# Kernel optimization log

Measured on AMD Instinct MI355X. Metric: run time of the kernel, lower is better.

Reference implementation:

```python
import jax, jax.numpy as jnp
import numpy as np

C = 256
HEAD_DIM = 8
N_HEAD = C // HEAD_DIM  # 32
GN_GROUPS = max(1, C // 32)  # 8
GN_EPS = 1e-5


def setup_inputs() -> dict:
    key = jax.random.key(0)
    ks = jax.random.split(key, 7)
    x = jax.random.normal(ks[0], (8, C, 32, 32), dtype=jnp.float32)
    gn_w = jax.random.normal(ks[1], (C,), dtype=jnp.float32) * 0.02 + 1.0
    gn_b = jax.random.normal(ks[2], (C,), dtype=jnp.float32) * 0.02
    qkv_w = jax.random.normal(ks[3], (3 * C, C), dtype=jnp.float32) / np.sqrt(C)
    qkv_b = jax.random.normal(ks[4], (3 * C,), dtype=jnp.float32) * 0.01
    out_w = jax.random.normal(ks[5], (C, C), dtype=jnp.float32) / np.sqrt(C)
    out_b = jax.random.normal(ks[6], (C,), dtype=jnp.float32) * 0.01
    return {"x": x, "gn_w": gn_w, "gn_b": gn_b, "qkv_w": qkv_w,
            "qkv_b": qkv_b, "out_w": out_w, "out_b": out_b}


def reference(x, gn_w, gn_b, qkv_w, qkv_b, out_w, out_b):
    n, c, h, w = x.shape
    hw = h * w
    # --- GroupNorm ---
    xg = x.reshape(n, GN_GROUPS, c // GN_GROUPS * hw)
    mu = jnp.mean(xg, axis=-1, keepdims=True)
    var = jnp.var(xg, axis=-1, keepdims=True)
    xn = ((xg - mu) * jax.lax.rsqrt(var + GN_EPS)).reshape(n, c, hw)
    xn = xn * gn_w[None, :, None] + gn_b[None, :, None]
    # --- QKV 1x1 conv ---
    qkv = jnp.einsum('oc,nct->not', qkv_w, xn) + qkv_b[None, :, None]  # [n,3c,hw]
    qkv = qkv.reshape(n, 3, N_HEAD, HEAD_DIM, hw)
    q, k, v = qkv[:, 0], qkv[:, 1], qkv[:, 2]  # each [n, heads, hd, hw]
    # --- attention over hw tokens ---
    scale = 1.0 / np.sqrt(HEAD_DIM)
    att = jnp.einsum('nhds,nhdt->nhst', q, k) * scale  # [n,heads,hw,hw]
    att = jax.nn.softmax(att, axis=-1)
    y = jnp.einsum('nhst,nhdt->nhds', att, v)  # [n,heads,hd,hw]
    y = y.reshape(n, c, hw)
    # --- output 1x1 conv + residual ---
    out = jnp.einsum('oc,nct->not', out_w, y) + out_b[None, :, None]
    return x + out.reshape(n, c, h, w)
```

## Files before the change

### kernel.cpp

```cpp
#include <hip/hip_runtime.h>
#include <hip/hip_bf16.h>
#include <math.h>


#define NBATCH 8
#define C 256
#define HW 1024
#define NHEAD 32
#define HDIM 8

typedef __bf16 bf16x8 __attribute__((ext_vector_type(8)));
typedef __bf16 bf16x4 __attribute__((ext_vector_type(4)));
typedef _Float16 f16x8 __attribute__((ext_vector_type(8)));
typedef _Float16 f16x4 __attribute__((ext_vector_type(4)));
typedef float floatx4 __attribute__((ext_vector_type(4)));
typedef float floatx16 __attribute__((ext_vector_type(16)));

#if __has_builtin(__builtin_amdgcn_exp2f)
#define EXP2F(x) __builtin_amdgcn_exp2f(x)
#else
#define EXP2F(x) exp2f(x)
#endif

#define SCALE_LOG2E 0.51013249662f

__global__ __launch_bounds__(256) void gn_stats_cvt_kernel(
    const float* __restrict__ x, float* __restrict__ stats,
    const float* __restrict__ qw, const float* __restrict__ ow,
    __bf16* __restrict__ wq, __bf16* __restrict__ wo)
{
    int blk = blockIdx.x;
    int tid = threadIdx.x;
    if (blk >= 512) {
        int id = (blk - 512) * 256 + tid;
        float4 v;
        __bf16* dst;
        if (id < 49152) { v = *(const float4*)&qw[id * 4]; dst = wq + id * 4; }
        else { v = *(const float4*)&ow[(id - 49152) * 4]; dst = wo + (id - 49152) * 4; }
        bf16x4 o = { (__bf16)v.x, (__bf16)v.y, (__bf16)v.z, (__bf16)v.w };
        *(bf16x4*)dst = o;
        return;
    }
    int part = blk & 7, ng = blk >> 3;
    const float4* xv = (const float4*)(x + ((size_t)ng * 32 + part * 4) * HW);
    float s = 0.f, ss = 0.f;
#pragma unroll
    for (int i = 0; i < 4; ++i) {
        float4 v = xv[tid + i * 256];
        s  += v.x + v.y + v.z + v.w;
        ss += v.x*v.x + v.y*v.y + v.z*v.z + v.w*v.w;
    }
#pragma unroll
    for (int o = 32; o; o >>= 1) { s += __shfl_xor(s, o); ss += __shfl_xor(ss, o); }
    __shared__ float rs[4], rss[4];
    int wave = tid >> 6, lane = tid & 63;
    if (lane == 0) { rs[wave] = s; rss[wave] = ss; }
    __syncthreads();
    if (tid == 0) {
        stats[blk * 2]     = rs[0] + rs[1] + rs[2] + rs[3];
        stats[blk * 2 + 1] = rss[0] + rss[1] + rss[2] + rss[3];
    }
}

__global__ __launch_bounds__(256) void gn_apply_kernel(
    const float* __restrict__ x, const float* __restrict__ w,
    const float* __restrict__ b, const float* __restrict__ stats,
    __bf16* __restrict__ xnT)
{
    int blk = blockIdx.x;
    int chunk = blk & 3, ng = blk >> 2;
    int n = ng >> 3, g = ng & 7;
    float s = 0.f, ss = 0.f;
#pragma unroll
    for (int p = 0; p < 8; ++p) {
        s  += stats[(ng * 8 + p) * 2];
        ss += stats[(ng * 8 + p) * 2 + 1];
    }
    const float invN = 1.0f / 32768.0f;
    float mean = s * invN;
    float var  = ss * invN - mean * mean;
    float rstd = rsqrtf(var + 1e-5f);
    const float* xp = x + ((size_t)ng * 32) * HW;
    int tid = threadIdx.x, t0 = chunk * 256;
    __shared__ __bf16 Lt[32][257];
#pragma unroll 8
    for (int c = 0; c < 32; ++c) {
        float wc = w[g * 32 + c] * rstd;
        float bc = b[g * 32 + c] - mean * wc;
        float v = xp[(size_t)c * HW + t0 + tid];
        Lt[c][tid] = (__bf16)(v * wc + bc);
    }
    __syncthreads();
    __bf16* xo = xnT + (size_t)n * HW * C + g * 32;
#pragma unroll
    for (int q = 0; q < 4; ++q) {
        bf16x8 o;
#pragma unroll
        for (int e = 0; e < 8; ++e) o[e] = Lt[q * 8 + e][tid];
        *(bf16x8*)&xo[(size_t)(t0 + tid) * C + q * 8] = o;
    }
}

__global__ __launch_bounds__(256) void gemm_qkv_kernel(
    const __bf16* __restrict__ W, const __bf16* __restrict__ Ball,
    const float* __restrict__ bias, _Float16* __restrict__ Qf,
    _Float16* __restrict__ Kf, __bf16* __restrict__ Vbf)
{
    int n = blockIdx.z;
    const __bf16* B = Ball + (size_t)n * HW * C;
    int om0 = blockIdx.y * 64, t0 = blockIdx.x * 128;
    __shared__ __bf16 As[64 * 32];
    __shared__ __bf16 Bs[128 * 32];
    int tid = threadIdx.x, lane = tid & 63, wave = tid >> 6;
    int l15 = lane & 15, quad = lane >> 4;
    int wm = (wave & 1) * 32, wn = (wave >> 1) * 64;
    int swq = (quad ^ (l15 & 3)) * 8;
    int arow = tid >> 2, aq = tid & 3;
    int sw = (aq ^ (arow & 3)) * 8;
    floatx4 acc[2][4] = {};
    for (int c0 = 0; c0 < C; c0 += 32) {
        bf16x8 av  = *(const bf16x8*)&W[(size_t)(om0 + arow) * C + c0 + aq * 8];
        bf16x8 bv0 = *(const bf16x8*)&B[(size_t)(t0 + arow) * C + c0 + aq * 8];
        bf16x8 bv1 = *(const bf16x8*)&B[(size_t)(t0 + 64 + arow) * C + c0 + aq * 8];
        __syncthreads();
        *(bf16x8*)&As[arow * 32 + sw] = av;
        *(bf16x8*)&Bs[arow * 32 + sw] = bv0;
        *(bf16x8*)&Bs[(arow + 64) * 32 + sw] = bv1;
        __syncthreads();
        bf16x8 af[2], bfr[4];
#pragma unroll
        for (int mi = 0; mi < 2; ++mi)
            af[mi] = *(const bf16x8*)&As[(wm + mi * 16 + l15) * 32 + swq];
#pragma unroll
        for (int ni = 0; ni < 4; ++ni)
            bfr[ni] = *(const bf16x8*)&Bs[(wn + ni * 16 + l15) * 32 + swq];
#pragma unroll
        for (int mi = 0; mi < 2; ++mi)
#pragma unroll
            for (int ni = 0; ni < 4; ++ni)
                acc[mi][ni] = __builtin_amdgcn_mfma_f32_16x16x32_bf16(
                    af[mi], bfr[ni], acc[mi][ni], 0, 0, 0);
    }
#pragma unroll
    for (int mi = 0; mi < 2; ++mi) {
        int obase = om0 + wm + mi * 16;
        int oq = obase + quad * 4;
        if (obase < 512) {
            int h  = (oq & 255) >> 3;
            int d0 = (quad & 1) * 4;
            _Float16* dst = (obase < 256 ? Qf : Kf);
            float mul = (obase < 256) ? SCALE_LOG2E : 1.0f;
#pragma unroll
            for (int ni = 0; ni < 4; ++ni) {
                int t = t0 + wn + ni * 16 + l15;
                f16x4 o;
#pragma unroll
                for (int r = 0; r < 4; ++r)
                    o[r] = (_Float16)((acc[mi][ni][r] + bias[oq + r]) * mul);
                *(f16x4*)&dst[(((size_t)(n * 32 + h)) * HW + t) * 8 + d0] = o;
            }
        } else {
            int cv = oq - 512;
#pragma unroll
            for (int ni = 0; ni < 4; ++ni) {
                int t = t0 + wn + ni * 16 + l15;
#pragma unroll
                for (int r = 0; r < 4; ++r)
                    Vbf[((size_t)(n * 256 + cv + r)) * HW + t] =
                        (__bf16)(acc[mi][ni][r] + bias[oq + r]);
            }
        }
    }
}

__global__ __launch_bounds__(256) void gemm_out_kernel(
    const __bf16* __restrict__ W, const __bf16* __restrict__ Ball,
    const float* __restrict__ bias, float* __restrict__ Call,
    const float* __restrict__ Rall)
{
    int n = blockIdx.z;
    const __bf16* B = Ball + (size_t)n * HW * C;
    float* Cp = Call + (size_t)n * C * HW;
    const float* R = Rall + (size_t)n * C * HW;
    int om0 = blockIdx.y * 64, t0 = blockIdx.x * 64;
    __shared__ __bf16 As[64 * 32];
    __shared__ __bf16 Bs[64 * 32];
    int tid = threadIdx.x, lane = tid & 63, wave = tid >> 6;
    int l15 = lane & 15, quad = lane >> 4;
    int wm = (wave & 1) * 32, wn = (wave >> 1) * 32;
    int swq = (quad ^ (l15 & 3)) * 8;
    int arow = tid >> 2, aq = tid & 3;
    int sw = (aq ^ (arow & 3)) * 8;
    floatx4 acc[2][2] = {};
    for (int c0 = 0; c0 < C; c0 += 32) {
        bf16x8 av = *(const bf16x8*)&W[(size_t)(om0 + arow) * C + c0 + aq * 8];
        bf16x8 bv = *(const bf16x8*)&B[(size_t)(t0 + arow) * C + c0 + aq * 8];
        __syncthreads();
        *(bf16x8*)&As[arow * 32 + sw] = av;
        *(bf16x8*)&Bs[arow * 32 + sw] = bv;
        __syncthreads();
        bf16x8 af[2], bfr[2];
#pragma unroll
        for (int mi = 0; mi < 2; ++mi)
            af[mi] = *(const bf16x8*)&As[(wm + mi * 16 + l15) * 32 + swq];
#pragma unroll
        for (int ni = 0; ni < 2; ++ni)
            bfr[ni] = *(const bf16x8*)&Bs[(wn + ni * 16 + l15) * 32 + swq];
#pragma unroll
        for (int mi = 0; mi < 2; ++mi)
#pragma unroll
            for (int ni = 0; ni < 2; ++ni)
                acc[mi][ni] = __builtin_amdgcn_mfma_f32_16x16x32_bf16(
                    af[mi], bfr[ni], acc[mi][ni], 0, 0, 0);
    }
#pragma unroll
    for (int mi = 0; mi < 2; ++mi) {
#pragma unroll
        for (int r = 0; r < 4; ++r) {
            int o = om0 + wm + mi * 16 + quad * 4 + r;
            float bb = bias[o];
#pragma unroll
            for (int ni = 0; ni < 2; ++ni) {
                int t = t0 + wn + ni * 16 + l15;
                Cp[(size_t)o * HW + t] = acc[mi][ni][r] + bb + R[(size_t)o * HW + t];
            }
        }
    }
}

__global__ __launch_bounds__(256, 4) void attn_kernel(
    const _Float16* __restrict__ Qf, const _Float16* __restrict__ Kf,
    const __bf16* __restrict__ Vg, __bf16* __restrict__ yT)
{
    int quarter = blockIdx.x & 3, h = (blockIdx.x >> 2) & 31, n = blockIdx.x >> 7;
    __shared__ alignas(16) _Float16 Kb[HW][8];
    __shared__ alignas(16) __bf16   Vb[9][HW + 8];
    int tid = threadIdx.x;
    const _Float16* kg = Kf + ((size_t)(n * 32 + h)) * HW * 8;
    const __bf16*   vg = Vg + ((size_t)(n * 256 + h * 8)) * HW;
#pragma unroll
    for (int i = 0; i < 4; ++i) {
        int row = tid + i * 256;
        *(f16x8*)&Kb[row][0] = *(const f16x8*)&kg[(size_t)row * 8];
    }
#pragma unroll
    for (int i = 0; i < 4; ++i) {
        int id = tid + i * 256;
        int d = id >> 7, t8 = (id & 127) * 8;
        *(bf16x8*)&Vb[d][t8] = *(const bf16x8*)&vg[(size_t)d * HW + t8];
    }
    if (tid < 128) {
        __bf16 one = (__bf16)1.0f;
        bf16x8 ones = { one, one, one, one, one, one, one, one };
        *(bf16x8*)&Vb[8][tid * 8] = ones;
    }
    int lane = tid & 63, wave = tid >> 6;
    int l31 = lane & 31, lhi = lane >> 5;
    int vrow = l31 < 9 ? l31 : (l31 & 7);
    const __bf16* vbase = &Vb[vrow][0];
    int tqb = quarter * 256 + wave * 64;
    const _Float16* qg = Qf + ((size_t)(n * 32 + h)) * HW * 8;
    f16x8 qf[2];
#pragma unroll
    for (int tau = 0; tau < 2; ++tau) {
        f16x8 qv = { 0, 0, 0, 0, 0, 0, 0, 0 };
        if (lhi == 0)
            qv = *(const f16x8*)&qg[(size_t)(tqb + tau * 32 + l31) * 8];
        qf[tau] = qv;
    }
    __syncthreads();
    floatx16 accG[2] = {};
    floatx16 zero16 = {};
    for (int tkt = 0; tkt < 32; ++tkt) {
        f16x8 kf = *(const f16x8*)&Kb[tkt * 32 + l31][0];
        int cb = tkt * 32 + lhi * 4;
        bf16x4 va0 = *(const bf16x4*)&vbase[cb];
        bf16x4 va1 = *(const bf16x4*)&vbase[cb + 8];
        bf16x4 va2 = *(const bf16x4*)&vbase[cb + 16];
        bf16x4 va3 = *(const bf16x4*)&vbase[cb + 24];
        bf16x8 vf0 = __builtin_shufflevector(va0, va1, 0, 1, 2, 3, 4, 5, 6, 7);
        bf16x8 vf1 = __builtin_shufflevector(va2, va3, 0, 1, 2, 3, 4, 5, 6, 7);
#pragma unroll
        for (int tau = 0; tau < 2; ++tau) {
            floatx16 sT = __builtin_amdgcn_mfma_f32_32x32x16_f16(
                kf, qf[tau], zero16, 0, 0, 0);
            __bf16 p[16];
#pragma unroll
            for (int r = 0; r < 16; ++r) p[r] = (__bf16)EXP2F(sT[r]);
            bf16x8 P0 = { p[0], p[1], p[2], p[3], p[4], p[5], p[6], p[7] };
            bf16x8 P1 = { p[8], p[9], p[10], p[11], p[12], p[13], p[14], p[15] };
            accG[tau] = __builtin_amdgcn_mfma_f32_32x32x16_bf16(
                vf0, P0, accG[tau], 0, 0, 0);
            accG[tau] = __builtin_amdgcn_mfma_f32_32x32x16_bf16(
                vf1, P1, accG[tau], 0, 0, 0);
        }
    }
    __bf16* yp = yT + (size_t)n * HW * C + h * HDIM + lhi * 4;
#pragma unroll
    for (int tau = 0; tau < 2; ++tau) {
        float own4 = accG[tau][4];
        float part4 = __shfl_xor(own4, 32);
        float lsum = lhi ? part4 : own4;
        float inv = 1.0f / lsum;
        bf16x4 o = { (__bf16)(accG[tau][0] * inv), (__bf16)(accG[tau][1] * inv),
                     (__bf16)(accG[tau][2] * inv), (__bf16)(accG[tau][3] * inv) };
        *(bf16x4*)&yp[(size_t)(tqb + tau * 32 + l31) * C] = o;
    }
}

extern "C" void kernel_launch(void* const* d_in, const int* in_sizes, int n_in,
                              void* d_out, int out_size, void* d_ws, size_t ws_size,
                              hipStream_t stream)
{
    const float* x     = (const float*)d_in[0];
    const float* gn_w  = (const float*)d_in[1];
    const float* gn_b  = (const float*)d_in[2];
    const float* qkv_w = (const float*)d_in[3];
    const float* qkv_b = (const float*)d_in[4];
    const float* out_w = (const float*)d_in[5];
    const float* out_b = (const float*)d_in[6];
    float* out = (float*)d_out;

    char* wsb = (char*)d_ws;
    __bf16*   xnT = (__bf16*)wsb;
    _Float16* Qf  = (_Float16*)(wsb + ((size_t)4 << 20));
    _Float16* Kf  = (_Float16*)(wsb + ((size_t)8 << 20));
    __bf16*   Vbf = (__bf16*)(wsb + ((size_t)12 << 20));
    __bf16*   yTp = (__bf16*)(wsb + ((size_t)16 << 20));
    __bf16*   wq  = (__bf16*)(wsb + ((size_t)20 << 20));
    __bf16*   wo  = wq + (size_t)3 * C * C;
    float*    st  = (float*)(wsb + ((size_t)21 << 20));

    gn_stats_cvt_kernel<<<768, 256, 0, stream>>>(x, st, qkv_w, out_w, wq, wo);
    gn_apply_kernel<<<256, 256, 0, stream>>>(x, gn_w, gn_b, st, xnT);
    gemm_qkv_kernel<<<dim3(8, 12, 8), 256, 0, stream>>>(wq, xnT, qkv_b,
                                                        Qf, Kf, Vbf);
    attn_kernel<<<1024, 256, 0, stream>>>(Qf, Kf, Vbf, yTp);
    gemm_out_kernel<<<dim3(16, 4, 8), 256, 0, stream>>>(wo, yTp, out_b, out, x);
}
```

Baseline: 125.4 us.

## Drop LDS staging in attention, read K/V from global and double block count

New measurement: 215.5 us. 1.72x slower.

```diff
diff --git a/kernel.cpp b/kernel.cpp
--- a/kernel.cpp
+++ b/kernel.cpp
@@ -27,12 +27,18 @@
 __global__ __launch_bounds__(256) void gn_stats_cvt_kernel(
     const float* __restrict__ x, float* __restrict__ stats,
     const float* __restrict__ qw, const float* __restrict__ ow,
-    __bf16* __restrict__ wq, __bf16* __restrict__ wo)
+    __bf16* __restrict__ wq, __bf16* __restrict__ wo,
+    __bf16* __restrict__ onesG)
 {
     int blk = blockIdx.x;
     int tid = threadIdx.x;
     if (blk >= 512) {
         int id = (blk - 512) * 256 + tid;
+        if (blk == 512 && tid < 128) {
+            __bf16 one = (__bf16)1.0f;
+            bf16x8 ones = { one, one, one, one, one, one, one, one };
+            *(bf16x8*)&onesG[tid * 8] = ones;
+        }
         float4 v;
         __bf16* dst;
         if (id < 49152) { v = *(const float4*)&qw[id * 4]; dst = wq + id * 4; }
@@ -228,84 +234,51 @@
     }
 }
 
-__global__ __launch_bounds__(256, 4) void attn_kernel(
+__global__ __launch_bounds__(256, 8) void attn_kernel(
     const _Float16* __restrict__ Qf, const _Float16* __restrict__ Kf,
-    const __bf16* __restrict__ Vg, __bf16* __restrict__ yT)
-{
-    int quarter = blockIdx.x & 3, h = (blockIdx.x >> 2) & 31, n = blockIdx.x >> 7;
-    __shared__ alignas(16) _Float16 Kb[HW][8];
-    __shared__ alignas(16) __bf16   Vb[9][HW + 8];
-    int tid = threadIdx.x;
+    const __bf16* __restrict__ Vg, const __bf16* __restrict__ onesG,
+    __bf16* __restrict__ yT)
+{
+    int eighth = blockIdx.x & 7, h = (blockIdx.x >> 3) & 31, n = blockIdx.x >> 8;
+    int tid = threadIdx.x, lane = tid & 63, wave = tid >> 6;
+    int l31 = lane & 31, lhi = lane >> 5;
     const _Float16* kg = Kf + ((size_t)(n * 32 + h)) * HW * 8;
     const __bf16*   vg = Vg + ((size_t)(n * 256 + h * 8)) * HW;
-#pragma unroll
-    for (int i = 0; i < 4; ++i) {
-        int row = tid + i * 256;
-        *(f16x8*)&Kb[row][0] = *(const f16x8*)&kg[(size_t)row * 8];
-    }
-#pragma unroll
-    for (int i = 0; i < 4; ++i) {
-        int id = tid + i * 256;
-        int d = id >> 7, t8 = (id & 127) * 8;
-        *(bf16x8*)&Vb[d][t8] = *(const bf16x8*)&vg[(size_t)d * HW + t8];
-    }
-    if (tid < 128) {
-        __bf16 one = (__bf16)1.0f;
-        bf16x8 ones = { one, one, one, one, one, one, one, one };
-        *(bf16x8*)&Vb[8][tid * 8] = ones;
-    }
-    int lane = tid & 63, wave = tid >> 6;
-    int l31 = lane & 31, lhi = lane >> 5;
-    int vrow = l31 < 9 ? l31 : (l31 & 7);
-    const __bf16* vbase = &Vb[vrow][0];
-    int tqb = quarter * 256 + wave * 64;
+    const __bf16* vrow = (l31 == 8) ? onesG : (vg + (size_t)(l31 & 7) * HW);
+    int tq0 = eighth * 128 + wave * 32;
     const _Float16* qg = Qf + ((size_t)(n * 32 + h)) * HW * 8;
-    f16x8 qf[2];
-#pragma unroll
-    for (int tau = 0; tau < 2; ++tau) {
-        f16x8 qv = { 0, 0, 0, 0, 0, 0, 0, 0 };
-        if (lhi == 0)
-            qv = *(const f16x8*)&qg[(size_t)(tqb + tau * 32 + l31) * 8];
-        qf[tau] = qv;
-    }
-    __syncthreads();
-    floatx16 accG[2] = {};
+    f16x8 qf = { 0, 0, 0, 0, 0, 0, 0, 0 };
+    if (lhi == 0)
+        qf = *(const f16x8*)&qg[(size_t)(tq0 + l31) * 8];
+    floatx16 acc = {};
     floatx16 zero16 = {};
     for (int tkt = 0; tkt < 32; ++tkt) {
-        f16x8 kf = *(const f16x8*)&Kb[tkt * 32 + l31][0];
+        f16x8 kf = *(const f16x8*)&kg[(size_t)(tkt * 32 + l31) * 8];
         int cb = tkt * 32 + lhi * 4;
-        bf16x4 va0 = *(const bf16x4*)&vbase[cb];
-        bf16x4 va1 = *(const bf16x4*)&vbase[cb + 8];
-        bf16x4 va2 = *(const bf16x4*)&vbase[cb + 16];
-        bf16x4 va3 = *(const bf16x4*)&vbase[cb + 24];
+        bf16x4 va0 = *(const bf16x4*)&vrow[cb];
+        bf16x4 va1 = *(const bf16x4*)&vrow[cb + 8];
+        bf16x4 va2 = *(const bf16x4*)&vrow[cb + 16];
+        bf16x4 va3 = *(const bf16x4*)&vrow[cb + 24];
         bf16x8 vf0 = __builtin_shufflevector(va0, va1, 0, 1, 2, 3, 4, 5, 6, 7);
         bf16x8 vf1 = __builtin_shufflevector(va2, va3, 0, 1, 2, 3, 4, 5, 6, 7);
-#pragma unroll
-        for (int tau = 0; tau < 2; ++tau) {
-            floatx16 sT = __builtin_amdgcn_mfma_f32_32x32x16_f16(
-                kf, qf[tau], zero16, 0, 0, 0);
-            __bf16 p[16];
-#pragma unroll
-            for (int r = 0; r < 16; ++r) p[r] = (__bf16)EXP2F(sT[r]);
-            bf16x8 P0 = { p[0], p[1], p[2], p[3], p[4], p[5], p[6], p[7] };
-            bf16x8 P1 = { p[8], p[9], p[10], p[11], p[12], p[13], p[14], p[15] };
-            accG[tau] = __builtin_amdgcn_mfma_f32_32x32x16_bf16(
-                vf0, P0, accG[tau], 0, 0, 0);
-            accG[tau] = __builtin_amdgcn_mfma_f32_32x32x16_bf16(
-                vf1, P1, accG[tau], 0, 0, 0);
-        }
+        floatx16 sT = __builtin_amdgcn_mfma_f32_32x32x16_f16(
+            kf, qf, zero16, 0, 0, 0);
+        __bf16 p[16];
+#pragma unroll
+        for (int r = 0; r < 16; ++r) p[r] = (__bf16)EXP2F(sT[r]);
+        bf16x8 P0 = { p[0], p[1], p[2], p[3], p[4], p[5], p[6], p[7] };
+        bf16x8 P1 = { p[8], p[9], p[10], p[11], p[12], p[13], p[14], p[15] };
+        acc = __builtin_amdgcn_mfma_f32_32x32x16_bf16(vf0, P0, acc, 0, 0, 0);
+        acc = __builtin_amdgcn_mfma_f32_32x32x16_bf16(vf1, P1, acc, 0, 0, 0);
     }
     __bf16* yp = yT + (size_t)n * HW * C + h * HDIM + lhi * 4;
-#pragma unroll
-    for (int tau = 0; tau < 2; ++tau) {
-        float own4 = accG[tau][4];
-        float part4 = __shfl_xor(own4, 32);
-        float lsum = lhi ? part4 : own4;
-        float inv = 1.0f / lsum;
-        bf16x4 o = { (__bf16)(accG[tau][0] * inv), (__bf16)(accG[tau][1] * inv),
-                     (__bf16)(accG[tau][2] * inv), (__bf16)(accG[tau][3] * inv) };
-        *(bf16x4*)&yp[(size_t)(tqb + tau * 32 + l31) * C] = o;
-    }
+    float own4 = acc[4];
+    float part4 = __shfl_xor(own4, 32);
+    float lsum = lhi ? part4 : own4;
+    float inv = 1.0f / lsum;
+    bf16x4 o = { (__bf16)(acc[0] * inv), (__bf16)(acc[1] * inv),
+                 (__bf16)(acc[2] * inv), (__bf16)(acc[3] * inv) };
+    *(bf16x4*)&yp[(size_t)(tq0 + l31) * C] = o;
 }
 
 extern "C" void kernel_launch(void* const* d_in, const int* in_sizes, int n_in,
@@ -330,11 +303,13 @@
     __bf16*   wq  = (__bf16*)(wsb + ((size_t)20 << 20));
     __bf16*   wo  = wq + (size_t)3 * C * C;
     float*    st  = (float*)(wsb + ((size_t)21 << 20));
-
-    gn_stats_cvt_kernel<<<768, 256, 0, stream>>>(x, st, qkv_w, out_w, wq, wo);
+    __bf16*   ones = (__bf16*)(wsb + ((size_t)21 << 20) + 8192);
+
+    gn_stats_cvt_kernel<<<768, 256, 0, stream>>>(x, st, qkv_w, out_w, wq, wo,
+                                                 ones);
     gn_apply_kernel<<<256, 256, 0, stream>>>(x, gn_w, gn_b, st, xnT);
     gemm_qkv_kernel<<<dim3(8, 12, 8), 256, 0, stream>>>(wq, xnT, qkv_b,
                                                         Qf, Kf, Vbf);
-    attn_kernel<<<1024, 256, 0, stream>>>(Qf, Kf, Vbf, yTp);
+    attn_kernel<<<2048, 256, 0, stream>>>(Qf, Kf, Vbf, ones, yTp);
     gemm_out_kernel<<<dim3(16, 4, 8), 256, 0, stream>>>(wo, yTp, out_b, out, x);
 }
```

## Load GEMM MFMA fragments directly from global memory, dropping LDS staging

Applied to the files above, without the earlier changes.

Result: slower. 137.9 us (+9.9%).

```diff
diff --git a/kernel.cpp b/kernel.cpp
--- a/kernel.cpp
+++ b/kernel.cpp
@@ -109,37 +109,33 @@
     int n = blockIdx.z;
     const __bf16* B = Ball + (size_t)n * HW * C;
     int om0 = blockIdx.y * 64, t0 = blockIdx.x * 128;
-    __shared__ __bf16 As[64 * 32];
-    __shared__ __bf16 Bs[128 * 32];
     int tid = threadIdx.x, lane = tid & 63, wave = tid >> 6;
     int l15 = lane & 15, quad = lane >> 4;
     int wm = (wave & 1) * 32, wn = (wave >> 1) * 64;
-    int swq = (quad ^ (l15 & 3)) * 8;
-    int arow = tid >> 2, aq = tid & 3;
-    int sw = (aq ^ (arow & 3)) * 8;
+    const __bf16* ap0 = &W[(size_t)(om0 + wm + l15) * C + quad * 8];
+    const __bf16* ap1 = ap0 + (size_t)16 * C;
+    const __bf16* bp0 = &B[(size_t)(t0 + wn + l15) * C + quad * 8];
+    const __bf16* bp1 = bp0 + (size_t)16 * C;
+    const __bf16* bp2 = bp0 + (size_t)32 * C;
+    const __bf16* bp3 = bp0 + (size_t)48 * C;
     floatx4 acc[2][4] = {};
-    for (int c0 = 0; c0 < C; c0 += 32) {
-        bf16x8 av  = *(const bf16x8*)&W[(size_t)(om0 + arow) * C + c0 + aq * 8];
-        bf16x8 bv0 = *(const bf16x8*)&B[(size_t)(t0 + arow) * C + c0 + aq * 8];
-        bf16x8 bv1 = *(const bf16x8*)&B[(size_t)(t0 + 64 + arow) * C + c0 + aq * 8];
-        __syncthreads();
-        *(bf16x8*)&As[arow * 32 + sw] = av;
-        *(bf16x8*)&Bs[arow * 32 + sw] = bv0;
-        *(bf16x8*)&Bs[(arow + 64) * 32 + sw] = bv1;
-        __syncthreads();
-        bf16x8 af[2], bfr[4];
-#pragma unroll
-        for (int mi = 0; mi < 2; ++mi)
-            af[mi] = *(const bf16x8*)&As[(wm + mi * 16 + l15) * 32 + swq];
-#pragma unroll
-        for (int ni = 0; ni < 4; ++ni)
-            bfr[ni] = *(const bf16x8*)&Bs[(wn + ni * 16 + l15) * 32 + swq];
-#pragma unroll
-        for (int mi = 0; mi < 2; ++mi)
-#pragma unroll
-            for (int ni = 0; ni < 4; ++ni)
-                acc[mi][ni] = __builtin_amdgcn_mfma_f32_16x16x32_bf16(
-                    af[mi], bfr[ni], acc[mi][ni], 0, 0, 0);
+#pragma unroll
+    for (int k = 0; k < 8; ++k) {
+        int c0 = k * 32;
+        bf16x8 af0 = *(const bf16x8*)&ap0[c0];
+        bf16x8 af1 = *(const bf16x8*)&ap1[c0];
+        bf16x8 bf0 = *(const bf16x8*)&bp0[c0];
+        bf16x8 bf1 = *(const bf16x8*)&bp1[c0];
+        bf16x8 bf2 = *(const bf16x8*)&bp2[c0];
+        bf16x8 bf3 = *(const bf16x8*)&bp3[c0];
+        acc[0][0] = __builtin_amdgcn_mfma_f32_16x16x32_bf16(af0, bf0, acc[0][0], 0, 0, 0);
+        acc[0][1] = __builtin_amdgcn_mfma_f32_16x16x32_bf16(af0, bf1, acc[0][1], 0, 0, 0);
+        acc[0][2] = __builtin_amdgcn_mfma_f32_16x16x32_bf16(af0, bf2, acc[0][2], 0, 0, 0);
+        acc[0][3] = __builtin_amdgcn_mfma_f32_16x16x32_bf16(af0, bf3, acc[0][3], 0, 0, 0);
+        acc[1][0] = __builtin_amdgcn_mfma_f32_16x16x32_bf16(af1, bf0, acc[1][0], 0, 0, 0);
+        acc[1][1] = __builtin_amdgcn_mfma_f32_16x16x32_bf16(af1, bf1, acc[1][1], 0, 0, 0);
+        acc[1][2] = __builtin_amdgcn_mfma_f32_16x16x32_bf16(af1, bf2, acc[1][2], 0, 0, 0);
+        acc[1][3] = __builtin_amdgcn_mfma_f32_16x16x32_bf16(af1, bf3, acc[1][3], 0, 0, 0);
     }
 #pragma unroll
     for (int mi = 0; mi < 2; ++mi) {
@@ -183,35 +179,25 @@
     float* Cp = Call + (size_t)n * C * HW;
     const float* R = Rall + (size_t)n * C * HW;
     int om0 = blockIdx.y * 64, t0 = blockIdx.x * 64;
-    __shared__ __bf16 As[64 * 32];
-    __shared__ __bf16 Bs[64 * 32];
     int tid = threadIdx.x, lane = tid & 63, wave = tid >> 6;
     int l15 = lane & 15, quad = lane >> 4;
     int wm = (wave & 1) * 32, wn = (wave >> 1) * 32;
-    int swq = (quad ^ (l15 & 3)) * 8;
-    int arow = tid >> 2, aq = tid & 3;
-    int sw = (aq ^ (arow & 3)) * 8;
+    const __bf16* ap0 = &W[(size_t)(om0 + wm + l15) * C + quad * 8];
+    const __bf16* ap1 = ap0 + (size_t)16 * C;
+    const __bf16* bp0 = &B[(size_t)(t0 + wn + l15) * C + quad * 8];
+    const __bf16* bp1 = bp0 + (size_t)16 * C;
     floatx4 acc[2][2] = {};
-    for (int c0 = 0; c0 < C; c0 += 32) {
-        bf16x8 av = *(const bf16x8*)&W[(size_t)(om0 + arow) * C + c0 + aq * 8];
-        bf16x8 bv = *(const bf16x8*)&B[(size_t)(t0 + arow) * C + c0 + aq * 8];
-        __syncthreads();
-        *(bf16x8*)&As[arow * 32 + sw] = av;
-        *(bf16x8*)&Bs[arow * 32 + sw] = bv;
-        __syncthreads();
-        bf16x8 af[2], bfr[2];
-#pragma unroll
-        for (int mi = 0; mi < 2; ++mi)
-            af[mi] = *(const bf16x8*)&As[(wm + mi * 16 + l15) * 32 + swq];
-#pragma unroll
-        for (int ni = 0; ni < 2; ++ni)
-            bfr[ni] = *(const bf16x8*)&Bs[(wn + ni * 16 + l15) * 32 + swq];
-#pragma unroll
-        for (int mi = 0; mi < 2; ++mi)
-#pragma unroll
-            for (int ni = 0; ni < 2; ++ni)
-                acc[mi][ni] = __builtin_amdgcn_mfma_f32_16x16x32_bf16(
-                    af[mi], bfr[ni], acc[mi][ni], 0, 0, 0);
+#pragma unroll
+    for (int k = 0; k < 8; ++k) {
+        int c0 = k * 32;
+        bf16x8 af0 = *(const bf16x8*)&ap0[c0];
+        bf16x8 af1 = *(const bf16x8*)&ap1[c0];
+        bf16x8 bf0 = *(const bf16x8*)&bp0[c0];
+        bf16x8 bf1 = *(const bf16x8*)&bp1[c0];
+        acc[0][0] = __builtin_amdgcn_mfma_f32_16x16x32_bf16(af0, bf0, acc[0][0], 0, 0, 0);
+        acc[0][1] = __builtin_amdgcn_mfma_f32_16x16x32_bf16(af0, bf1, acc[0][1], 0, 0, 0);
+        acc[1][0] = __builtin_amdgcn_mfma_f32_16x16x32_bf16(af1, bf0, acc[1][0], 0, 0, 0);
+        acc[1][1] = __builtin_amdgcn_mfma_f32_16x16x32_bf16(af1, bf1, acc[1][1], 0, 0, 0);
     }
 #pragma unroll
     for (int mi = 0; mi < 2; ++mi) {
```
